# Optimization experiments

Hardware: AMD Instinct MI355X
Metric: run time of the kernel (lower is better)

## Reference

```python
import jax, jax.numpy as jnp
import numpy as np

B, CQ, CC, COUT, H, W = 32, 256, 3, 256, 32, 32
INTER = CQ // 2
HC, WC = 224, 224
EPS = 1e-5


def setup_inputs() -> dict:
    key = jax.random.key(0)
    ks = jax.random.split(key, 12)
    s = lambda fan_in: 1.0 / np.sqrt(fan_in)
    return {
        "query_feat": jax.random.normal(ks[0], (B, CQ, H, W), jnp.float32),
        "context_feat": jax.random.normal(ks[1], (B, CC, HC, WC), jnp.float32),
        "Wq": jax.random.uniform(ks[2], (INTER, CQ), jnp.float32, -s(CQ), s(CQ)),
        "bq": jax.random.uniform(ks[3], (INTER,), jnp.float32, -s(CQ), s(CQ)),
        "Wk": jax.random.uniform(ks[4], (INTER, CC), jnp.float32, -s(CC), s(CC)),
        "bk": jax.random.uniform(ks[5], (INTER,), jnp.float32, -s(CC), s(CC)),
        "Wv": jax.random.uniform(ks[6], (CQ, CC), jnp.float32, -s(CC), s(CC)),
        "bv": jax.random.uniform(ks[7], (CQ,), jnp.float32, -s(CC), s(CC)),
        "Wp": jax.random.uniform(ks[8], (COUT, CQ), jnp.float32, -s(CQ), s(CQ)),
        "bp": jax.random.uniform(ks[9], (COUT,), jnp.float32, -s(CQ), s(CQ)),
        "gamma": jnp.ones((COUT,), jnp.float32),
        "beta": jnp.zeros((COUT,), jnp.float32),
    }


def _conv1x1(x, Wmat, b):
    # x: [B,Cin,H,W], Wmat: [Cout,Cin] -> [B,Cout,H,W]
    return jnp.einsum("oc,bchw->bohw", Wmat, x) + b[None, :, None, None]


def reference(query_feat, context_feat, Wq, bq, Wk, bk, Wv, bv, Wp, bp, gamma, beta):
    Bn, Cq, Hn, Wn = query_feat.shape
    HWn = Hn * Wn
    # bilinear resize, align_corners=False, no antialias (matches F.interpolate)
    ctx = jax.image.resize(context_feat, (Bn, context_feat.shape[1], Hn, Wn),
                           method="linear", antialias=False)
    q = _conv1x1(query_feat, Wq, bq).reshape(Bn, -1, HWn)   # [B,inter,HW]
    k = _conv1x1(ctx, Wk, bk).reshape(Bn, -1, HWn)          # [B,inter,HW]
    v = _conv1x1(ctx, Wv, bv).reshape(Bn, Cq, HWn)          # [B,Cq,HW]
    scores = jnp.einsum("bci,bcj->bij", q, k)               # [B,HW,HW]
    probs = jax.nn.softmax(scores, axis=-1)
    # attended_v[b,c,i] = sum_j v[b,c,j] * probs[b,i,j]
    attended = jnp.einsum("bcj,bij->bci", v, probs).reshape(Bn, Cq, Hn, Wn)
    fused = _conv1x1(query_feat + attended, Wp, bp)         # [B,Cout,H,W]
    # GroupNorm with 1 group: normalize over (C,H,W) per sample
    mu = jnp.mean(fused, axis=(1, 2, 3), keepdims=True)
    var = jnp.var(fused, axis=(1, 2, 3), keepdims=True)
    normed = (fused - mu) * jax.lax.rsqrt(var + EPS)
    return normed * gamma[None, :, None, None] + beta[None, :, None, None]
```

## Files before the change

### kernel.cpp

```cpp
#include <hip/hip_runtime.h>
#include <hip/hip_bf16.h>

#define WS_M4    0
#define WS_M0    1024
#define WS_G4    1056
#define WS_BSUM  2080
#define WS_BSSQ  2112
#define WS_BAR   2144
#define WS_WPB   2176
#define WS_CTX   34944

typedef __attribute__((ext_vector_type(8))) short short8;
typedef __attribute__((ext_vector_type(4))) float floatx4;

__device__ inline unsigned short f2bf(float x) {
    unsigned u = __float_as_uint(x);
    return (unsigned short)((u + 0x7FFFu + ((u >> 16) & 1u)) >> 16);
}

__global__ __launch_bounds__(256) void sca_pre(
    const float* __restrict__ Wq, const float* __restrict__ bq,
    const float* __restrict__ Wk, const float* __restrict__ bk,
    const float* __restrict__ Wv, const float* __restrict__ bv,
    const float* __restrict__ Wp, const float* __restrict__ bp,
    const float* __restrict__ ctxin, float* __restrict__ ws)
{
    int tid = threadIdx.x;
    int blk = blockIdx.x;
    if (blk < 4) {
        __shared__ float WkL[384];
        __shared__ float bqL[128];
        __shared__ float redM[4][64][3];
        int o0 = blk << 6;
        if (tid < 128) bqL[tid] = bq[tid];
        for (int idx = tid; idx < 384; idx += 256) WkL[idx] = Wk[idx];
        __syncthreads();
        int o64 = tid & 63, cg = tid >> 6;
        float m0v = 0.f, m1v = 0.f, m2v = 0.f;
        for (int c0 = cg * 32; c0 < cg * 32 + 32; c0 += 16) {
            float q[16];
#pragma unroll
            for (int j = 0; j < 16; ++j) q[j] = Wq[(c0 + j) * 256 + o0 + o64];
#pragma unroll
            for (int j = 0; j < 16; ++j) {
                int c = c0 + j;
                m0v = fmaf(WkL[c * 3 + 0], q[j], m0v);
                m1v = fmaf(WkL[c * 3 + 1], q[j], m1v);
                m2v = fmaf(WkL[c * 3 + 2], q[j], m2v);
            }
        }
        redM[cg][o64][0] = m0v; redM[cg][o64][1] = m1v; redM[cg][o64][2] = m2v;
        __syncthreads();
        if (tid < 64) {
            float r0 = redM[0][tid][0] + redM[1][tid][0] + redM[2][tid][0] + redM[3][tid][0];
            float r1 = redM[0][tid][1] + redM[1][tid][1] + redM[2][tid][1] + redM[3][tid][1];
            float r2 = redM[0][tid][2] + redM[1][tid][2] + redM[2][tid][2] + redM[3][tid][2];
            ((float4*)(ws + WS_M4))[o0 + tid] = make_float4(r0, r1, r2, 0.f);
        }
        if (blk == 0) {
            if (tid < 3) {
                float s = 0.f;
                for (int c = 0; c < 128; ++c) s = fmaf(WkL[c * 3 + tid], bqL[c], s);
                ws[WS_M0 + tid] = s;
            }
            if (tid < 65) ws[WS_BSUM + tid] = 0.f;
        }
    } else if (blk < 36) {
        __shared__ float WvL[768];
        __shared__ float bvL[256];
        for (int idx = tid; idx < 768; idx += 256) WvL[idx] = Wv[idx];
        bvL[tid] = bv[tid];
        __syncthreads();
        int idx = (blk - 4) * 2048 + tid * 8;
        int o = idx >> 8;
        int kt = (tid & 31) >> 2, quad = tid & 3;
        const float4* s = (const float4*)(Wp + idx);
        float4 x0 = s[0], x1 = s[1];
        uint4 v;
        v.x = (unsigned)f2bf(x0.x) | ((unsigned)f2bf(x0.y) << 16);
        v.y = (unsigned)f2bf(x0.z) | ((unsigned)f2bf(x0.w) << 16);
        v.z = (unsigned)f2bf(x1.x) | ((unsigned)f2bf(x1.y) << 16);
        v.w = (unsigned)f2bf(x1.z) | ((unsigned)f2bf(x1.w) << 16);
        int slot = (((o >> 4) * 8 + kt) * 64) + quad * 16 + (o & 15);
        ((uint4*)((unsigned short*)(ws + WS_WPB)))[slot] = v;
        int c0 = idx & 255;
        float xv[8] = {x0.x, x0.y, x0.z, x0.w, x1.x, x1.y, x1.z, x1.w};
        float g0 = 0.f, g1 = 0.f, g2 = 0.f, gb = 0.f;
#pragma unroll
        for (int j = 0; j < 8; ++j) {
            int c = c0 + j;
            g0 = fmaf(xv[j], WvL[c * 3 + 0], g0);
            g1 = fmaf(xv[j], WvL[c * 3 + 1], g1);
            g2 = fmaf(xv[j], WvL[c * 3 + 2], g2);
            gb = fmaf(xv[j], bvL[c], gb);
        }
#pragma unroll
        for (int off = 1; off < 32; off <<= 1) {
            g0 += __shfl_xor(g0, off);
            g1 += __shfl_xor(g1, off);
            g2 += __shfl_xor(g2, off);
            gb += __shfl_xor(gb, off);
        }
        if ((tid & 31) == 0)
            ((float4*)(ws + WS_G4))[o] = make_float4(g0, g1, g2, gb + bp[o]);
    } else {
        int g = (blk - 36) * 256 + tid;
        int b = g >> 10, j = g & 1023;
        int y = j >> 5, x = j & 31;
        const float* src = ctxin + (size_t)b * 150528;
        int p = (7 * y + 3) * 224 + (7 * x + 3);
        ((float4*)(ws + WS_CTX))[g] =
            make_float4(src[p], src[p + 50176], src[p + 100352], 0.f);
    }
}

__global__ __launch_bounds__(1024, 4) void sca_mega(const float* __restrict__ Q,
                                                    float* __restrict__ ws,
                                                    const float* __restrict__ gamma,
                                                    const float* __restrict__ beta,
                                                    float* __restrict__ out)
{
    __shared__ float4 cs4[1024];
    __shared__ float4 Ms4[256];
    __shared__ uint4 QL[2048];
    __shared__ float red[16][64][7];
    __shared__ float4 av4[128];
    __shared__ float4 cps[128];
    __shared__ float sred[34];

    int tid = threadIdx.x;
    int blk = blockIdx.x;
    int b  = blk >> 3;
    int i0 = (blk & 7) << 7;
    int lane = tid & 63, w = tid >> 6;
    int m = lane & 15, quad = lane >> 4;

    const float* Qbase = Q + ((size_t)b << 18) + i0 + (lane << 1);
    float2 qv[4];
#pragma unroll
    for (int s = 0; s < 4; ++s)
        qv[s] = *(const float2*)(Qbase + ((size_t)(w * 4 + s) << 10));
    {
        const float4* cg4 = ((const float4*)(ws + WS_CTX)) + ((size_t)b << 10);
        cs4[tid] = cg4[tid];
        if (tid < 256) Ms4[tid] = ((const float4*)(ws + WS_M4))[tid];
    }
    __syncthreads();

    const short8* Apack = (const short8*)((const unsigned short*)(ws + WS_WPB));
    floatx4 acc[8] = {};
    float ap[6] = {};

    for (int c = 0; c < 4; ++c) {
#pragma unroll
        for (int s = 0; s < 4; ++s) {
            float4 mv = Ms4[c * 64 + w * 4 + s];
            ap[0] = fmaf(mv.x, qv[s].x, ap[0]); ap[1] = fmaf(mv.x, qv[s].y, ap[1]);
            ap[2] = fmaf(mv.y, qv[s].x, ap[2]); ap[3] = fmaf(mv.y, qv[s].y, ap[3]);
            ap[4] = fmaf(mv.z, qv[s].x, ap[4]); ap[5] = fmaf(mv.z, qv[s].y, ap[5]);
        }
        unsigned lo0 = (unsigned)f2bf(qv[0].x) | ((unsigned)f2bf(qv[1].x) << 16);
        unsigned hi0 = (unsigned)f2bf(qv[2].x) | ((unsigned)f2bf(qv[3].x) << 16);
        unsigned lo1 = (unsigned)f2bf(qv[0].y) | ((unsigned)f2bf(qv[1].y) << 16);
        unsigned hi1 = (unsigned)f2bf(qv[2].y) | ((unsigned)f2bf(qv[3].y) << 16);
        {
            uint2* QB = (uint2*)(QL + (c & 1) * 1024);
            int i = lane << 1;
            int gs = (w >> 1) ^ (i & 7) ^ ((i >> 2) & 7);
            QB[(i * 8 + gs) * 2 + (w & 1)] = make_uint2(lo0, hi0);
            i |= 1;
            gs = (w >> 1) ^ (i & 7) ^ ((i >> 2) & 7);
            QB[(i * 8 + gs) * 2 + (w & 1)] = make_uint2(lo1, hi1);
        }
        if (c < 3) {
#pragma unroll
            for (int s = 0; s < 4; ++s)
                qv[s] = *(const float2*)(Qbase + ((size_t)((c + 1) * 64 + w * 4 + s) << 10));
        }
        __syncthreads();
        const short8* QBs = (const short8*)(QL + (c & 1) * 1024);
#pragma unroll
        for (int kk = 0; kk < 2; ++kk) {
            short8 af = Apack[(w * 8 + c * 2 + kk) * 64 + lane];
#pragma unroll
            for (int it = 0; it < 8; ++it) {
                int i = it * 16 + m;
                int g = kk * 4 + quad;
                int gs = g ^ (i & 7) ^ ((i >> 2) & 7);
                short8 bf = QBs[i * 8 + gs];
                acc[it] = __builtin_amdgcn_mfma_f32_16x16x32_bf16(
                    af, bf, acc[it], 0, 0, 0);
            }
        }
    }

#pragma unroll
    for (int j = 0; j < 6; ++j) red[w][lane][j] = ap[j];
    __syncthreads();
    if (tid < 128) {
        int ln = tid >> 1, e = tid & 1;
        float r0 = ws[WS_M0 + 0], r1 = ws[WS_M0 + 1], r2 = ws[WS_M0 + 2];
#pragma unroll
        for (int wv = 0; wv < 16; ++wv) {
            r0 += red[wv][ln][0 + e];
            r1 += red[wv][ln][2 + e];
            r2 += red[wv][ln][4 + e];
        }
        av4[tid] = make_float4(r0, r1, r2, 0.f);
    }
    __syncthreads();

    {
        int sl = tid & 7, qg = tid >> 3;
        float4 a = av4[qg];
        float sh = 6.0f * (fabsf(a.x) + fabsf(a.y) + fabsf(a.z));
        float d = 0.f, s0 = 0.f, s1 = 0.f, s2 = 0.f;
#pragma unroll 4
        for (int jj = 0; jj < 128; ++jj) {
            float4 cv = cs4[(jj << 3) + sl];
            float sc = fmaf(a.x, cv.x, fmaf(a.y, cv.y, a.z * cv.z));
            float e = __expf(sc - sh);
            d += e;
            s0 = fmaf(e, cv.x, s0);
            s1 = fmaf(e, cv.y, s1);
            s2 = fmaf(e, cv.z, s2);
        }
        d  += __shfl_xor(d, 1);  d  += __shfl_xor(d, 2);  d  += __shfl_xor(d, 4);
        s0 += __shfl_xor(s0, 1); s0 += __shfl_xor(s0, 2); s0 += __shfl_xor(s0, 4);
        s1 += __shfl_xor(s1, 1); s1 += __shfl_xor(s1, 2); s1 += __shfl_xor(s1, 4);
        s2 += __shfl_xor(s2, 1); s2 += __shfl_xor(s2, 2); s2 += __shfl_xor(s2, 4);
        if (sl == 0) {
            float inv = 1.0f / d;
            cps[qg] = make_float4(s0 * inv, s1 * inv, s2 * inv, 0.f);
        }
    }
    __syncthreads();

    const floatx4* G4 = (const floatx4*)(ws + WS_G4);
    floatx4 gv[4];
    float gaw[4], btw[4];
#pragma unroll
    for (int r = 0; r < 4; ++r) {
        int o = w * 16 + quad * 4 + r;
        gv[r] = G4[o];
        gaw[r] = gamma[o];
        btw[r] = beta[o];
    }
    float lsum = 0.f, lssq = 0.f;
#pragma unroll
    for (int it = 0; it < 8; ++it) {
        float4 cp = cps[it * 16 + m];
#pragma unroll
        for (int r = 0; r < 4; ++r) {
            float v = acc[it][r]
                    + gv[r][0] * cp.x + gv[r][1] * cp.y + gv[r][2] * cp.z + gv[r][3];
            acc[it][r] = v;
            lsum += v; lssq = fmaf(v, v, lssq);
        }
    }
#pragma unroll
    for (int off = 32; off > 0; off >>= 1) {
        lsum += __shfl_down(lsum, off);
        lssq += __shfl_down(lssq, off);
    }
    if (lane == 0) { sred[w] = lsum; sred[16 + w] = lssq; }
    __syncthreads();

    if (tid == 0) {
        float s = 0.f, q2 = 0.f;
#pragma unroll
        for (int j = 0; j < 16; ++j) { s += sred[j]; q2 += sred[16 + j]; }
        atomicAdd(ws + WS_BSUM + b, s);
        atomicAdd(ws + WS_BSSQ + b, q2);
        __threadfence();
        int* bar = (int*)(ws + WS_BAR);
        atomicAdd(bar, 1);
        while (atomicAdd(bar, 0) < 256) __builtin_amdgcn_s_sleep(2);
        sred[32] = atomicAdd(ws + WS_BSUM + b, 0.0f);
        sred[33] = atomicAdd(ws + WS_BSSQ + b, 0.0f);
    }
    __syncthreads();

    const float inv_n = 1.0f / 262144.0f;
    float mean = sred[32] * inv_n;
    float var  = fmaf(sred[33], inv_n, -mean * mean);
    float rs = rsqrtf(var + 1e-5f);
    float gm[4], gb2[4];
#pragma unroll
    for (int r = 0; r < 4; ++r) {
        gm[r] = gaw[r] * rs;
        gb2[r] = fmaf(-mean, gm[r], btw[r]);
    }
#pragma unroll
    for (int it = 0; it < 8; ++it) {
#pragma unroll
        for (int r = 0; r < 4; ++r) {
            int o = w * 16 + quad * 4 + r;
            out[(((size_t)(b * 256 + o)) << 10) + i0 + it * 16 + m] =
                fmaf(acc[it][r], gm[r], gb2[r]);
        }
    }
}

extern "C" void kernel_launch(void* const* d_in, const int* in_sizes, int n_in,
                              void* d_out, int out_size, void* d_ws, size_t ws_size,
                              hipStream_t stream)
{
    const float* Q     = (const float*)d_in[0];
    const float* ctxf  = (const float*)d_in[1];
    const float* Wq    = (const float*)d_in[2];
    const float* bq    = (const float*)d_in[3];
    const float* Wk    = (const float*)d_in[4];
    const float* bk    = (const float*)d_in[5];
    const float* Wv    = (const float*)d_in[6];
    const float* bv    = (const float*)d_in[7];
    const float* Wp    = (const float*)d_in[8];
    const float* bp    = (const float*)d_in[9];
    const float* gamma = (const float*)d_in[10];
    const float* beta  = (const float*)d_in[11];
    float* ws  = (float*)d_ws;
    float* out = (float*)d_out;

    sca_pre <<<164, 256, 0, stream>>>(Wq, bq, Wk, bk, Wv, bv, Wp, bp, ctxf, ws);
    sca_mega<<<256, 1024, 0, stream>>>(Q, ws, gamma, beta, out);
}
```

Measured before the change: 148.2 us.

## Replace in-kernel grid barrier with a separate GroupNorm kernel

```diff
diff --git a/kernel.cpp b/kernel.cpp
--- a/kernel.cpp
+++ b/kernel.cpp
@@ -116,8 +116,6 @@
 
 __global__ __launch_bounds__(1024, 4) void sca_mega(const float* __restrict__ Q,
                                                     float* __restrict__ ws,
-                                                    const float* __restrict__ gamma,
-                                                    const float* __restrict__ beta,
                                                     float* __restrict__ out)
 {
     __shared__ float4 cs4[1024];
@@ -126,7 +124,7 @@
     __shared__ float red[16][64][7];
     __shared__ float4 av4[128];
     __shared__ float4 cps[128];
-    __shared__ float sred[34];
+    __shared__ float sred[32];
 
     int tid = threadIdx.x;
     int blk = blockIdx.x;
@@ -238,23 +236,18 @@
 
     const floatx4* G4 = (const floatx4*)(ws + WS_G4);
     floatx4 gv[4];
-    float gaw[4], btw[4];
-#pragma unroll
-    for (int r = 0; r < 4; ++r) {
-        int o = w * 16 + quad * 4 + r;
-        gv[r] = G4[o];
-        gaw[r] = gamma[o];
-        btw[r] = beta[o];
-    }
+#pragma unroll
+    for (int r = 0; r < 4; ++r) gv[r] = G4[w * 16 + quad * 4 + r];
     float lsum = 0.f, lssq = 0.f;
 #pragma unroll
     for (int it = 0; it < 8; ++it) {
         float4 cp = cps[it * 16 + m];
 #pragma unroll
         for (int r = 0; r < 4; ++r) {
+            int o = w * 16 + quad * 4 + r;
             float v = acc[it][r]
                     + gv[r][0] * cp.x + gv[r][1] * cp.y + gv[r][2] * cp.z + gv[r][3];
-            acc[it][r] = v;
+            out[(((size_t)(b * 256 + o)) << 10) + i0 + it * 16 + m] = v;
             lsum += v; lssq = fmaf(v, v, lssq);
         }
     }
@@ -265,40 +258,38 @@
     }
     if (lane == 0) { sred[w] = lsum; sred[16 + w] = lssq; }
     __syncthreads();
-
     if (tid == 0) {
         float s = 0.f, q2 = 0.f;
 #pragma unroll
         for (int j = 0; j < 16; ++j) { s += sred[j]; q2 += sred[16 + j]; }
         atomicAdd(ws + WS_BSUM + b, s);
         atomicAdd(ws + WS_BSSQ + b, q2);
-        __threadfence();
-        int* bar = (int*)(ws + WS_BAR);
-        atomicAdd(bar, 1);
-        while (atomicAdd(bar, 0) < 256) __builtin_amdgcn_s_sleep(2);
-        sred[32] = atomicAdd(ws + WS_BSUM + b, 0.0f);
-        sred[33] = atomicAdd(ws + WS_BSSQ + b, 0.0f);
-    }
-    __syncthreads();
-
+    }
+}
+
+__global__ __launch_bounds__(256) void sca_norm(float* __restrict__ out,
+                                                const float* __restrict__ ws,
+                                                const float* __restrict__ gamma,
+                                                const float* __restrict__ beta)
+{
     const float inv_n = 1.0f / 262144.0f;
-    float mean = sred[32] * inv_n;
-    float var  = fmaf(sred[33], inv_n, -mean * mean);
-    float rs = rsqrtf(var + 1e-5f);
-    float gm[4], gb2[4];
 #pragma unroll
     for (int r = 0; r < 4; ++r) {
-        gm[r] = gaw[r] * rs;
-        gb2[r] = fmaf(-mean, gm[r], btw[r]);
-    }
-#pragma unroll
-    for (int it = 0; it < 8; ++it) {
-#pragma unroll
-        for (int r = 0; r < 4; ++r) {
-            int o = w * 16 + quad * 4 + r;
-            out[(((size_t)(b * 256 + o)) << 10) + i0 + it * 16 + m] =
-                fmaf(acc[it][r], gm[r], gb2[r]);
-        }
+        size_t idx = (size_t)r * 524288 + (size_t)blockIdx.x * 256 + threadIdx.x;
+        float4 v = ((const float4*)out)[idx];
+        size_t base = idx << 2;
+        int b = (int)(base >> 18);
+        int o = (int)((base >> 10) & 255);
+        float mean = ws[WS_BSUM + b] * inv_n;
+        float var  = fmaf(ws[WS_BSSQ + b], inv_n, -mean * mean);
+        float rs = rsqrtf(var + 1e-5f);
+        float ga = gamma[o] * rs;
+        float be = fmaf(-mean, ga, beta[o]);
+        v.x = fmaf(v.x, ga, be);
+        v.y = fmaf(v.y, ga, be);
+        v.z = fmaf(v.z, ga, be);
+        v.w = fmaf(v.w, ga, be);
+        ((float4*)out)[idx] = v;
     }
 }
 
@@ -321,6 +312,7 @@
     float* ws  = (float*)d_ws;
     float* out = (float*)d_out;
 
-    sca_pre <<<164, 256, 0, stream>>>(Wq, bq, Wk, bk, Wv, bv, Wp, bp, ctxf, ws);
-    sca_mega<<<256, 1024, 0, stream>>>(Q, ws, gamma, beta, out);
-}
+    sca_pre <<<164,  256, 0, stream>>>(Wq, bq, Wk, bk, Wv, bv, Wp, bp, ctxf, ws);
+    sca_mega<<<256, 1024, 0, stream>>>(Q, ws, out);
+    sca_norm<<<2048, 256, 0, stream>>>(out, ws, gamma, beta);
+}
```

After: 148.6 us. Within noise of the previous version (+0.3%).
